# Optimization experiments

Measured on AMD Instinct MI355X. Metric: run time of the kernel, lower is better.

The kernel has to match this reference:

```python
import jax, jax.numpy as jnp
import numpy as np

EPS = 1e-5

def _layernorm(x, g, b):
    m = jnp.mean(x, axis=-1, keepdims=True)
    v = jnp.mean(jnp.square(x - m), axis=-1, keepdims=True)
    return (x - m) * jax.lax.rsqrt(v + EPS) * g + b

def setup_inputs() -> dict:
    key = jax.random.key(0)
    ks = jax.random.split(key, 4)
    B, N, D = 8, 256, 128
    h = jax.random.normal(ks[0], (B, N, D), dtype=jnp.float32)
    adj_J = jax.random.normal(ks[1], (B, N, N), dtype=jnp.float32)
    W_msg = jax.random.normal(ks[2], (D, 2 * D + 1), dtype=jnp.float32) * 0.05
    W_upd = jax.random.normal(ks[3], (D, 2 * D), dtype=jnp.float32) * 0.05
    return {
        "h": h, "adj_J": adj_J,
        "W_msg": W_msg, "b_msg": jnp.zeros((D,), jnp.float32),
        "g_msg": jnp.ones((D,), jnp.float32), "beta_msg": jnp.zeros((D,), jnp.float32),
        "W_upd": W_upd, "b_upd": jnp.zeros((D,), jnp.float32),
        "g_upd": jnp.ones((D,), jnp.float32), "beta_upd": jnp.zeros((D,), jnp.float32),
    }

def reference(h, adj_J, W_msg, b_msg, g_msg, beta_msg, W_upd, b_upd, g_upd, beta_upd):
    B, N, D = h.shape
    # Split msg Linear weight: cat([h_target, h_source, J]) @ W.T is separable.
    Wt = W_msg[:, :D]        # acts on h_target (node i, dim 1)
    Ws = W_msg[:, D:2 * D]   # acts on h_source (node j, dim 2)
    wJ = W_msg[:, 2 * D]     # acts on scalar J
    # pre[b,i,j,e] = h[b,i]@Wt.T + h[b,j]@Ws.T + J[b,i,j]*wJ + b
    pre = (jnp.einsum('bid,ed->bie', h, Wt)[:, :, None, :]
           + jnp.einsum('bjd,ed->bje', h, Ws)[:, None, :, :]
           + adj_J[..., None] * wJ
           + b_msg)
    messages = jax.nn.silu(_layernorm(pre, g_msg, beta_msg))  # (B,N,N,D)
    # mask out self-messages (j == i) then sum over sources j
    idx = jnp.arange(N)
    agg = jnp.sum(messages, axis=2) - messages[:, idx, idx, :]  # (B,N,D)
    upd_pre = (jnp.einsum('bnd,ed->bne', h, W_upd[:, :D])
               + jnp.einsum('bnd,ed->bne', agg, W_upd[:, D:])
               + b_upd)
    dh = jax.nn.silu(_layernorm(upd_pre, g_upd, beta_upd))
    return h + dh
```

## Files before the change

### kernel.cpp

```cpp
#include <hip/hip_runtime.h>

#define BB 8
#define NN 256
#define DD 128
#define SW 257
#define SU 256
#define EPSV 1e-5f

__device__ __forceinline__ float wave_reduce_add(float v) {
#pragma unroll
  for (int off = 32; off > 0; off >>= 1) v += __shfl_xor(v, off, 64);
  return v;
}

__global__ __launch_bounds__(256) void k_proj(
    const float* __restrict__ h, const float* __restrict__ Wm,
    const float* __restrict__ bmsg, const float* __restrict__ Wu,
    float* __restrict__ u, float* __restrict__ s,
    float* __restrict__ rowA, float* __restrict__ rowB,
    float* __restrict__ rowD2, float* __restrict__ rowE2,
    float* __restrict__ wtilv, float* __restrict__ wut) {
  const int blk = blockIdx.x;
  const int b = blk >> 6;
  const int r0 = (blk & 63) * 4;
  const int tid = threadIdx.x;
  const int half = tid >> 7, e = tid & 127;
  const int wv = tid >> 6, lane = tid & 63;

  __shared__ float hs[4][DD];
  __shared__ float pS[4][4], pw[2], pQ[4][4], pD[4][4];

  const float* hb = h + (size_t)(b * NN + r0) * DD;
  if (tid < DD) {
#pragma unroll
    for (int r = 0; r < 4; ++r) hs[r][e] = hb[r * DD + e];
  }
  if (tid >= DD && tid < DD + 64) {
    const int i = blk * 64 + (tid - DD);
    const int d = i >> 7, e2 = i & 127;
    wut[i] = Wu[(size_t)e2 * SU + d];
  }
  __syncthreads();

  float acc[4];
  const float bm = (half == 0) ? bmsg[e] : 0.f;
#pragma unroll
  for (int r = 0; r < 4; ++r) acc[r] = bm;

  const float* wr = Wm + (size_t)e * SW + half * DD;
#pragma unroll 8
  for (int k = 0; k < DD; k += 4) {
    const float4 w4 = *(const float4*)(wr + k);
#pragma unroll
    for (int r = 0; r < 4; ++r) {
      const float4 hv = *(const float4*)(&hs[r][k]);
      acc[r] = fmaf(hv.x, w4.x, acc[r]);
      acc[r] = fmaf(hv.y, w4.y, acc[r]);
      acc[r] = fmaf(hv.z, w4.z, acc[r]);
      acc[r] = fmaf(hv.w, w4.w, acc[r]);
    }
  }

  const float we = Wm[(size_t)e * SW + 2 * DD];
#pragma unroll
  for (int r = 0; r < 4; ++r) {
    const float sm = wave_reduce_add(acc[r]);
    if (lane == 0) pS[wv][r] = sm;
  }
  {
    const float sw = wave_reduce_add(we);
    if (lane == 0 && wv < 2) pw[wv] = sw;
  }
  __syncthreads();

  const int b2 = half * 2;
  const float muw = (pw[0] + pw[1]) * (1.f / DD);
  const float wtil = we - muw;
  float c[4];
#pragma unroll
  for (int r = 0; r < 4; ++r)
    c[r] = acc[r] - (pS[b2][r] + pS[b2 + 1][r]) * (1.f / DD);

  float* outp = (half == 0 ? u : s) + (size_t)(b * NN + r0) * DD;
#pragma unroll
  for (int r = 0; r < 4; ++r) outp[r * DD + e] = c[r];
  if (blk == 0 && half == 0) wtilv[e] = wtil;

#pragma unroll
  for (int r = 0; r < 4; ++r) {
    const float q = wave_reduce_add(c[r] * c[r]);
    const float dd = wave_reduce_add(c[r] * wtil);
    if (lane == 0) { pQ[wv][r] = q; pD[wv][r] = dd; }
  }
  __syncthreads();
  if (tid < 4) {
    const int row = b * NN + r0 + tid;
    rowA[row]  = pQ[0][tid] + pQ[1][tid];
    rowD2[row] = 2.f * (pD[0][tid] + pD[1][tid]);
    rowB[row]  = pQ[2][tid] + pQ[3][tid];
    rowE2[row] = 2.f * (pD[2][tid] + pD[3][tid]);
  }
}

__global__ __launch_bounds__(256) void k_msgfused(
    const float* __restrict__ h, const float* __restrict__ u,
    const float* __restrict__ s, const float* __restrict__ adj,
    const float* __restrict__ rowA, const float* __restrict__ rowB,
    const float* __restrict__ rowD2, const float* __restrict__ rowE2,
    const float* __restrict__ wtilv, const float* __restrict__ g,
    const float* __restrict__ be, const float* __restrict__ wut,
    const float* __restrict__ bu, const float* __restrict__ gu,
    const float* __restrict__ beu, float* __restrict__ out) {
  const int blk = blockIdx.x;
  const int b = blk >> 7, ip = blk & 127;
  const int i0 = 2 * ip, i1 = i0 + 1;
  const int tid = threadIdx.x, lane = tid & 63, wv = tid >> 6;
  const int bNN = b * NN;

  __shared__ __align__(16) float st_[32 * 132];
  __shared__ __align__(16) float upair_[2 * DD];
  __shared__ __align__(16) float hrow_[2 * DD];
  __shared__ float2 pak0[32], pak1[32];
  __shared__ float pm[2][2], pq[2][2];

  {
    const int ii = tid >> 7, e = tid & 127;
    upair_[ii * DD + e] = u[(size_t)(bNN + i0 + ii) * DD + e];
    hrow_[ii * DD + e]  = h[(size_t)(bNN + i0 + ii) * DD + e];
  }
  const float2 wt2 = *(const float2*)(wtilv + 2 * lane);
  const float2 g2  = *(const float2*)(g + 2 * lane);
  const float2 be2 = *(const float2*)(be + 2 * lane);
  const float C = wave_reduce_add(fmaf(wt2.x, wt2.x, wt2.y * wt2.y));
  const float A0 = rowA[bNN + i0], A1 = rowA[bNN + i1];
  const float D20 = rowD2[bNN + i0], D21 = rowD2[bNN + i1];
  __syncthreads();
  const float2 uu0 = *(const float2*)(&upair_[2 * lane]);
  const float2 uu1 = *(const float2*)(&upair_[DD + 2 * lane]);

  float accA0 = 0.f, accA1 = 0.f, accB0 = 0.f, accB1 = 0.f;
  const float* sb = s + (size_t)bNN * DD;

  for (int tile = 0; tile < 8; ++tile) {
    const int t0 = tile * 32;
    __syncthreads();
    {
      const int r = tid >> 5, c4 = (tid & 31) * 4;
#pragma unroll
      for (int p = 0; p < 4; ++p) {
        const int row = p * 8 + r;
        *(float4*)(&st_[row * 132 + c4]) =
            *(const float4*)(sb + (size_t)(t0 + row) * DD + c4);
      }
    }
    __syncthreads();
    {
      const int j = tid >> 3, seg = tid & 7, k0 = seg * 16;
      float d0 = 0.f, d1 = 0.f;
#pragma unroll
      for (int k = 0; k < 16; k += 4) {
        const float4 sv = *(const float4*)(&st_[j * 132 + k0 + k]);
        const float4 u0v = *(const float4*)(&upair_[k0 + k]);
        const float4 u1v = *(const float4*)(&upair_[DD + k0 + k]);
        d0 = fmaf(sv.x, u0v.x, d0); d0 = fmaf(sv.y, u0v.y, d0);
        d0 = fmaf(sv.z, u0v.z, d0); d0 = fmaf(sv.w, u0v.w, d0);
        d1 = fmaf(sv.x, u1v.x, d1); d1 = fmaf(sv.y, u1v.y, d1);
        d1 = fmaf(sv.z, u1v.z, d1); d1 = fmaf(sv.w, u1v.w, d1);
      }
#pragma unroll
      for (int m = 1; m < 8; m <<= 1) {
        d0 += __shfl_xor(d0, m, 64);
        d1 += __shfl_xor(d1, m, 64);
      }
      if (seg == 0) {
        const int jg = t0 + j;
        const float Bj = rowB[bNN + jg], E2j = rowE2[bNN + jg];
        const float a0 = adj[(size_t)(bNN + i0) * NN + jg];
        const float a1 = adj[(size_t)(bNN + i1) * NN + jg];
        const float q0 = fmaf(a0, fmaf(a0, C, D20 + E2j), A0 + Bj + 2.f * d0);
        const float q1 = fmaf(a1, fmaf(a1, C, D21 + E2j), A1 + Bj + 2.f * d1);
        pak0[j] = make_float2(a0, __builtin_amdgcn_rsqf(fmaf(q0, 1.f / DD, EPSV)));
        pak1[j] = make_float2(a1, __builtin_amdgcn_rsqf(fmaf(q1, 1.f / DD, EPSV)));
      }
    }
    __syncthreads();
    for (int jj = wv; jj < 32; jj += 4) {
      const int jg = t0 + jj;
      const float2 ss = *(const float2*)(&st_[jj * 132 + 2 * lane]);
      const float sx0 = uu0.x + ss.x, sx1 = uu0.y + ss.y;
      const float tx0 = uu1.x + ss.x, tx1 = uu1.y + ss.y;
      if (jg != i0) {
        const float2 p = pak0[jj];
        const float x0 = fmaf(p.x, wt2.x, sx0);
        const float x1 = fmaf(p.x, wt2.y, sx1);
        const float y0 = fmaf(x0 * p.y, g2.x, be2.x);
        const float y1 = fmaf(x1 * p.y, g2.y, be2.y);
        accA0 = fmaf(y0, __builtin_amdgcn_rcpf(1.f + __expf(-y0)), accA0);
        accA1 = fmaf(y1, __builtin_amdgcn_rcpf(1.f + __expf(-y1)), accA1);
      }
      if (jg != i1) {
        const float2 p = pak1[jj];
        const float x0 = fmaf(p.x, wt2.x, tx0);
        const float x1 = fmaf(p.x, wt2.y, tx1);
        const float y0 = fmaf(x0 * p.y, g2.x, be2.x);
        const float y1 = fmaf(x1 * p.y, g2.y, be2.y);
        accB0 = fmaf(y0, __builtin_amdgcn_rcpf(1.f + __expf(-y0)), accB0);
        accB1 = fmaf(y1, __builtin_amdgcn_rcpf(1.f + __expf(-y1)), accB1);
      }
    }
  }

  __syncthreads();
  *(float2*)(&st_[(wv * 2 + 0) * DD + 2 * lane]) = make_float2(accA0, accA1);
  *(float2*)(&st_[(wv * 2 + 1) * DD + 2 * lane]) = make_float2(accB0, accB1);
  __syncthreads();
  {
    const int ii = tid >> 7, e = tid & 127;
    st_[(8 + ii) * DD + e] = st_[(0 * 2 + ii) * DD + e] +
                             st_[(1 * 2 + ii) * DD + e] +
                             st_[(2 * 2 + ii) * DD + e] +
                             st_[(3 * 2 + ii) * DD + e];
  }
  __syncthreads();

  const int half = tid >> 7, e = tid & 127;
  float v0 = (half == 0) ? bu[e] : 0.f;
  float v1 = v0;
  {
    const float* xin = (half == 0) ? hrow_ : &st_[8 * DD];
    const float* wcol = wut + (size_t)half * DD * DD + e;
#pragma unroll 8
    for (int k = 0; k < DD; ++k) {
      const float w = wcol[(size_t)k * DD];
      v0 = fmaf(xin[k], w, v0);
      v1 = fmaf(xin[DD + k], w, v1);
    }
  }
  if (half == 1) { upair_[e] = v0; upair_[DD + e] = v1; }
  __syncthreads();
  if (half == 0) {
    v0 += upair_[e];
    v1 += upair_[DD + e];
    const float sm0 = wave_reduce_add(v0), sq0 = wave_reduce_add(v0 * v0);
    const float sm1 = wave_reduce_add(v1), sq1 = wave_reduce_add(v1 * v1);
    if (lane == 0) {
      pm[wv][0] = sm0; pq[wv][0] = sq0;
      pm[wv][1] = sm1; pq[wv][1] = sq1;
    }
  }
  __syncthreads();
  if (half == 0) {
    const float ge = gu[e], bee = beu[e];
    {
      const float mean = (pm[0][0] + pm[1][0]) * (1.f / DD);
      const float var = (pq[0][0] + pq[1][0]) * (1.f / DD) - mean * mean;
      const float rs = __builtin_amdgcn_rsqf(var + EPSV);
      const float y = fmaf((v0 - mean) * rs, ge, bee);
      const float sg = __builtin_amdgcn_rcpf(1.f + __expf(-y));
      out[(size_t)(bNN + i0) * DD + e] = hrow_[e] + y * sg;
    }
    {
      const float mean = (pm[0][1] + pm[1][1]) * (1.f / DD);
      const float var = (pq[0][1] + pq[1][1]) * (1.f / DD) - mean * mean;
      const float rs = __builtin_amdgcn_rsqf(var + EPSV);
      const float y = fmaf((v1 - mean) * rs, ge, bee);
      const float sg = __builtin_amdgcn_rcpf(1.f + __expf(-y));
      out[(size_t)(bNN + i1) * DD + e] = hrow_[DD + e] + y * sg;
    }
  }
}

extern "C" void kernel_launch(void* const* d_in, const int* in_sizes, int n_in,
                              void* d_out, int out_size, void* d_ws, size_t ws_size,
                              hipStream_t stream) {
  const float* h    = (const float*)d_in[0];
  const float* adj  = (const float*)d_in[1];
  const float* Wm   = (const float*)d_in[2];
  const float* bmsg = (const float*)d_in[3];
  const float* gmsg = (const float*)d_in[4];
  const float* bemsg= (const float*)d_in[5];
  const float* Wu   = (const float*)d_in[6];
  const float* bupd = (const float*)d_in[7];
  const float* gupd = (const float*)d_in[8];
  const float* beupd= (const float*)d_in[9];
  float* out = (float*)d_out;

  float* ws    = (float*)d_ws;
  float* u     = ws;
  float* s     = u + BB * NN * DD;
  float* rowA  = s + BB * NN * DD;
  float* rowB  = rowA + BB * NN;
  float* rowD2 = rowB + BB * NN;
  float* rowE2 = rowD2 + BB * NN;
  float* wtilv = rowE2 + BB * NN;
  float* wut   = wtilv + DD;

  k_proj<<<512, 256, 0, stream>>>(h, Wm, bmsg, Wu, u, s, rowA, rowB, rowD2,
                                  rowE2, wtilv, wut);
  k_msgfused<<<1024, 256, 0, stream>>>(h, u, s, adj, rowA, rowB, rowD2, rowE2,
                                       wtilv, gmsg, bemsg, wut, bupd, gupd,
                                       beupd, out);
}
```

Baseline: 56.30 us.

## Double-buffer source tiles with register prefetch in fused message kernel

```diff
diff --git a/kernel.cpp b/kernel.cpp
--- a/kernel.cpp
+++ b/kernel.cpp
@@ -102,7 +102,7 @@
   }
 }
 
-__global__ __launch_bounds__(256) void k_msgfused(
+__global__ __launch_bounds__(256) void k_msgdb(
     const float* __restrict__ h, const float* __restrict__ u,
     const float* __restrict__ s, const float* __restrict__ adj,
     const float* __restrict__ rowA, const float* __restrict__ rowB,
@@ -117,10 +117,10 @@
   const int tid = threadIdx.x, lane = tid & 63, wv = tid >> 6;
   const int bNN = b * NN;
 
-  __shared__ __align__(16) float st_[32 * 132];
+  __shared__ __align__(16) float st_[2][32 * 132];
   __shared__ __align__(16) float upair_[2 * DD];
   __shared__ __align__(16) float hrow_[2 * DD];
-  __shared__ float2 pak0[32], pak1[32];
+  __shared__ float2 pak0[2][32], pak1[2][32];
   __shared__ float pm[2][2], pq[2][2];
 
   {
@@ -138,88 +138,120 @@
   const float2 uu0 = *(const float2*)(&upair_[2 * lane]);
   const float2 uu1 = *(const float2*)(&upair_[DD + 2 * lane]);
 
+  const int j8 = tid >> 3, seg = tid & 7, k0 = seg * 16;
+  const float* srcbase = s + (size_t)(bNN + j8) * DD + k0;
+  float4 ra, rb, rc, rd;
+
+#define DOTS_WRITE(BUF, T) do {                                               \
+    float d0 = 0.f, d1 = 0.f;                                                 \
+    const float4 ua0 = *(const float4*)(&upair_[k0]);                         \
+    const float4 ua1 = *(const float4*)(&upair_[k0 + 4]);                     \
+    const float4 ua2 = *(const float4*)(&upair_[k0 + 8]);                     \
+    const float4 ua3 = *(const float4*)(&upair_[k0 + 12]);                    \
+    const float4 ub0 = *(const float4*)(&upair_[DD + k0]);                    \
+    const float4 ub1 = *(const float4*)(&upair_[DD + k0 + 4]);                \
+    const float4 ub2 = *(const float4*)(&upair_[DD + k0 + 8]);                \
+    const float4 ub3 = *(const float4*)(&upair_[DD + k0 + 12]);               \
+    d0 = fmaf(ra.x, ua0.x, d0); d0 = fmaf(ra.y, ua0.y, d0);                   \
+    d0 = fmaf(ra.z, ua0.z, d0); d0 = fmaf(ra.w, ua0.w, d0);                   \
+    d0 = fmaf(rb.x, ua1.x, d0); d0 = fmaf(rb.y, ua1.y, d0);                   \
+    d0 = fmaf(rb.z, ua1.z, d0); d0 = fmaf(rb.w, ua1.w, d0);                   \
+    d0 = fmaf(rc.x, ua2.x, d0); d0 = fmaf(rc.y, ua2.y, d0);                   \
+    d0 = fmaf(rc.z, ua2.z, d0); d0 = fmaf(rc.w, ua2.w, d0);                   \
+    d0 = fmaf(rd.x, ua3.x, d0); d0 = fmaf(rd.y, ua3.y, d0);                   \
+    d0 = fmaf(rd.z, ua3.z, d0); d0 = fmaf(rd.w, ua3.w, d0);                   \
+    d1 = fmaf(ra.x, ub0.x, d1); d1 = fmaf(ra.y, ub0.y, d1);                   \
+    d1 = fmaf(ra.z, ub0.z, d1); d1 = fmaf(ra.w, ub0.w, d1);                   \
+    d1 = fmaf(rb.x, ub1.x, d1); d1 = fmaf(rb.y, ub1.y, d1);                   \
+    d1 = fmaf(rb.z, ub1.z, d1); d1 = fmaf(rb.w, ub1.w, d1);                   \
+    d1 = fmaf(rc.x, ub2.x, d1); d1 = fmaf(rc.y, ub2.y, d1);                   \
+    d1 = fmaf(rc.z, ub2.z, d1); d1 = fmaf(rc.w, ub2.w, d1);                   \
+    d1 = fmaf(rd.x, ub3.x, d1); d1 = fmaf(rd.y, ub3.y, d1);                   \
+    d1 = fmaf(rd.z, ub3.z, d1); d1 = fmaf(rd.w, ub3.w, d1);                   \
+    float* dst = &st_[BUF][j8 * 132 + k0];                                    \
+    *(float4*)(dst)      = ra; *(float4*)(dst + 4)  = rb;                     \
+    *(float4*)(dst + 8)  = rc; *(float4*)(dst + 12) = rd;                     \
+    d0 += __shfl_xor(d0, 1, 64); d1 += __shfl_xor(d1, 1, 64);                 \
+    d0 += __shfl_xor(d0, 2, 64); d1 += __shfl_xor(d1, 2, 64);                 \
+    d0 += __shfl_xor(d0, 4, 64); d1 += __shfl_xor(d1, 4, 64);                 \
+    if (seg == 0) {                                                           \
+      const int jg = (T) * 32 + j8;                                           \
+      const float Bj = rowB[bNN + jg], E2j = rowE2[bNN + jg];                 \
+      const float a0 = adj[(size_t)(bNN + i0) * NN + jg];                     \
+      const float a1 = adj[(size_t)(bNN + i1) * NN + jg];                     \
+      const float q0 = fmaf(a0, fmaf(a0, C, D20 + E2j), A0 + Bj + 2.f * d0);  \
+      const float q1 = fmaf(a1, fmaf(a1, C, D21 + E2j), A1 + Bj + 2.f * d1);  \
+      pak0[BUF][j8] = make_float2(a0,                                         \
+          __builtin_amdgcn_rsqf(fmaf(q0, 1.f / DD, EPSV)));                   \
+      pak1[BUF][j8] = make_float2(a1,                                         \
+          __builtin_amdgcn_rsqf(fmaf(q1, 1.f / DD, EPSV)));                   \
+    }                                                                         \
+  } while (0)
+
+  {
+    const float* p = srcbase;
+    ra = *(const float4*)(p);     rb = *(const float4*)(p + 4);
+    rc = *(const float4*)(p + 8); rd = *(const float4*)(p + 12);
+  }
+  DOTS_WRITE(0, 0);
+  __syncthreads();
+
   float accA0 = 0.f, accA1 = 0.f, accB0 = 0.f, accB1 = 0.f;
-  const float* sb = s + (size_t)bNN * DD;
-
-  for (int tile = 0; tile < 8; ++tile) {
-    const int t0 = tile * 32;
-    __syncthreads();
+  int cur = 0;
+
+  for (int t = 0; t < 8; ++t) {
+    if (t < 7) {
+      const float* p = srcbase + (size_t)(t + 1) * 32 * DD;
+      ra = *(const float4*)(p);     rb = *(const float4*)(p + 4);
+      rc = *(const float4*)(p + 8); rd = *(const float4*)(p + 12);
+    }
     {
-      const int r = tid >> 5, c4 = (tid & 31) * 4;
-#pragma unroll
-      for (int p = 0; p < 4; ++p) {
-        const int row = p * 8 + r;
-        *(float4*)(&st_[row * 132 + c4]) =
-            *(const float4*)(sb + (size_t)(t0 + row) * DD + c4);
+      const float* stc = st_[cur];
+      const float2* p0 = pak0[cur];
+      const float2* p1 = pak1[cur];
+      const int t0 = t * 32;
+      for (int jj = wv; jj < 32; jj += 4) {
+        const int jg = t0 + jj;
+        const float2 ss = *(const float2*)(&stc[jj * 132 + 2 * lane]);
+        const float sx0 = uu0.x + ss.x, sx1 = uu0.y + ss.y;
+        const float tx0 = uu1.x + ss.x, tx1 = uu1.y + ss.y;
+        if (jg != i0) {
+          const float2 p = p0[jj];
+          const float x0 = fmaf(p.x, wt2.x, sx0);
+          const float x1 = fmaf(p.x, wt2.y, sx1);
+          const float y0 = fmaf(x0 * p.y, g2.x, be2.x);
+          const float y1 = fmaf(x1 * p.y, g2.y, be2.y);
+          accA0 = fmaf(y0, __builtin_amdgcn_rcpf(1.f + __expf(-y0)), accA0);
+          accA1 = fmaf(y1, __builtin_amdgcn_rcpf(1.f + __expf(-y1)), accA1);
+        }
+        if (jg != i1) {
+          const float2 p = p1[jj];
+          const float x0 = fmaf(p.x, wt2.x, tx0);
+          const float x1 = fmaf(p.x, wt2.y, tx1);
+          const float y0 = fmaf(x0 * p.y, g2.x, be2.x);
+          const float y1 = fmaf(x1 * p.y, g2.y, be2.y);
+          accB0 = fmaf(y0, __builtin_amdgcn_rcpf(1.f + __expf(-y0)), accB0);
+          accB1 = fmaf(y1, __builtin_amdgcn_rcpf(1.f + __expf(-y1)), accB1);
+        }
       }
     }
-    __syncthreads();
-    {
-      const int j = tid >> 3, seg = tid & 7, k0 = seg * 16;
-      float d0 = 0.f, d1 = 0.f;
-#pragma unroll
-      for (int k = 0; k < 16; k += 4) {
-        const float4 sv = *(const float4*)(&st_[j * 132 + k0 + k]);
-        const float4 u0v = *(const float4*)(&upair_[k0 + k]);
-        const float4 u1v = *(const float4*)(&upair_[DD + k0 + k]);
-        d0 = fmaf(sv.x, u0v.x, d0); d0 = fmaf(sv.y, u0v.y, d0);
-        d0 = fmaf(sv.z, u0v.z, d0); d0 = fmaf(sv.w, u0v.w, d0);
-        d1 = fmaf(sv.x, u1v.x, d1); d1 = fmaf(sv.y, u1v.y, d1);
-        d1 = fmaf(sv.z, u1v.z, d1); d1 = fmaf(sv.w, u1v.w, d1);
-      }
-#pragma unroll
-      for (int m = 1; m < 8; m <<= 1) {
-        d0 += __shfl_xor(d0, m, 64);
-        d1 += __shfl_xor(d1, m, 64);
-      }
-      if (seg == 0) {
-        const int jg = t0 + j;
-        const float Bj = rowB[bNN + jg], E2j = rowE2[bNN + jg];
-        const float a0 = adj[(size_t)(bNN + i0) * NN + jg];
-        const float a1 = adj[(size_t)(bNN + i1) * NN + jg];
-        const float q0 = fmaf(a0, fmaf(a0, C, D20 + E2j), A0 + Bj + 2.f * d0);
-        const float q1 = fmaf(a1, fmaf(a1, C, D21 + E2j), A1 + Bj + 2.f * d1);
-        pak0[j] = make_float2(a0, __builtin_amdgcn_rsqf(fmaf(q0, 1.f / DD, EPSV)));
-        pak1[j] = make_float2(a1, __builtin_amdgcn_rsqf(fmaf(q1, 1.f / DD, EPSV)));
-      }
-    }
-    __syncthreads();
-    for (int jj = wv; jj < 32; jj += 4) {
-      const int jg = t0 + jj;
-      const float2 ss = *(const float2*)(&st_[jj * 132 + 2 * lane]);
-      const float sx0 = uu0.x + ss.x, sx1 = uu0.y + ss.y;
-      const float tx0 = uu1.x + ss.x, tx1 = uu1.y + ss.y;
-      if (jg != i0) {
-        const float2 p = pak0[jj];
-        const float x0 = fmaf(p.x, wt2.x, sx0);
-        const float x1 = fmaf(p.x, wt2.y, sx1);
-        const float y0 = fmaf(x0 * p.y, g2.x, be2.x);
-        const float y1 = fmaf(x1 * p.y, g2.y, be2.y);
-        accA0 = fmaf(y0, __builtin_amdgcn_rcpf(1.f + __expf(-y0)), accA0);
-        accA1 = fmaf(y1, __builtin_amdgcn_rcpf(1.f + __expf(-y1)), accA1);
-      }
-      if (jg != i1) {
-        const float2 p = pak1[jj];
-        const float x0 = fmaf(p.x, wt2.x, tx0);
-        const float x1 = fmaf(p.x, wt2.y, tx1);
-        const float y0 = fmaf(x0 * p.y, g2.x, be2.x);
-        const float y1 = fmaf(x1 * p.y, g2.y, be2.y);
-        accB0 = fmaf(y0, __builtin_amdgcn_rcpf(1.f + __expf(-y0)), accB0);
-        accB1 = fmaf(y1, __builtin_amdgcn_rcpf(1.f + __expf(-y1)), accB1);
-      }
-    }
-  }
-
-  __syncthreads();
-  *(float2*)(&st_[(wv * 2 + 0) * DD + 2 * lane]) = make_float2(accA0, accA1);
-  *(float2*)(&st_[(wv * 2 + 1) * DD + 2 * lane]) = make_float2(accB0, accB1);
+    if (t < 7) {
+      DOTS_WRITE(cur ^ 1, t + 1);
+      __syncthreads();
+      cur ^= 1;
+    }
+  }
+
+  __syncthreads();
+  *(float2*)(&st_[0][(wv * 2 + 0) * DD + 2 * lane]) = make_float2(accA0, accA1);
+  *(float2*)(&st_[0][(wv * 2 + 1) * DD + 2 * lane]) = make_float2(accB0, accB1);
   __syncthreads();
   {
     const int ii = tid >> 7, e = tid & 127;
-    st_[(8 + ii) * DD + e] = st_[(0 * 2 + ii) * DD + e] +
-                             st_[(1 * 2 + ii) * DD + e] +
-                             st_[(2 * 2 + ii) * DD + e] +
-                             st_[(3 * 2 + ii) * DD + e];
+    st_[0][(8 + ii) * DD + e] = st_[0][(0 + ii) * DD + e] +
+                                st_[0][(2 + ii) * DD + e] +
+                                st_[0][(4 + ii) * DD + e] +
+                                st_[0][(6 + ii) * DD + e];
   }
   __syncthreads();
 
@@ -227,7 +259,7 @@
   float v0 = (half == 0) ? bu[e] : 0.f;
   float v1 = v0;
   {
-    const float* xin = (half == 0) ? hrow_ : &st_[8 * DD];
+    const float* xin = (half == 0) ? hrow_ : &st_[0][8 * DD];
     const float* wcol = wut + (size_t)half * DD * DD + e;
 #pragma unroll 8
     for (int k = 0; k < DD; ++k) {
@@ -297,7 +329,7 @@
 
   k_proj<<<512, 256, 0, stream>>>(h, Wm, bmsg, Wu, u, s, rowA, rowB, rowD2,
                                   rowE2, wtilv, wut);
-  k_msgfused<<<1024, 256, 0, stream>>>(h, u, s, adj, rowA, rowB, rowD2, rowE2,
-                                       wtilv, gmsg, bemsg, wut, bupd, gupd,
-                                       beupd, out);
+  k_msgdb<<<1024, 256, 0, stream>>>(h, u, s, adj, rowA, rowB, rowD2, rowE2,
+                                    wtilv, gmsg, bemsg, wut, bupd, gupd,
+                                    beupd, out);
 }
```

Result: no change. 56.48 us (+0.3%).

## Replace shared-memory tiling of source rows with register prefetch in message kernel

Applied to the files above, without the earlier changes.

```diff
diff --git a/kernel.cpp b/kernel.cpp
--- a/kernel.cpp
+++ b/kernel.cpp
@@ -6,6 +6,8 @@
 #define SW 257
 #define SU 256
 #define EPSV 1e-5f
+#define LOG2E 1.4426950408889634f
+#define LN2F 0.6931471805599453f
 
 __device__ __forceinline__ float wave_reduce_add(float v) {
 #pragma unroll
@@ -102,7 +104,7 @@
   }
 }
 
-__global__ __launch_bounds__(256) void k_msgfused(
+__global__ __launch_bounds__(256) void k_msgreg(
     const float* __restrict__ h, const float* __restrict__ u,
     const float* __restrict__ s, const float* __restrict__ adj,
     const float* __restrict__ rowA, const float* __restrict__ rowB,
@@ -115,12 +117,14 @@
   const int b = blk >> 7, ip = blk & 127;
   const int i0 = 2 * ip, i1 = i0 + 1;
   const int tid = threadIdx.x, lane = tid & 63, wv = tid >> 6;
+  const int seg = lane & 7, jloc = lane >> 3;
+  const int jrow = wv * 8 + jloc;
   const int bNN = b * NN;
 
-  __shared__ __align__(16) float st_[32 * 132];
   __shared__ __align__(16) float upair_[2 * DD];
   __shared__ __align__(16) float hrow_[2 * DD];
-  __shared__ float2 pak0[32], pak1[32];
+  __shared__ __align__(16) float4 pakr_[NN];
+  __shared__ __align__(16) float sacc_[10 * DD];
   __shared__ float pm[2][2], pq[2][2];
 
   {
@@ -128,98 +132,116 @@
     upair_[ii * DD + e] = u[(size_t)(bNN + i0 + ii) * DD + e];
     hrow_[ii * DD + e]  = h[(size_t)(bNN + i0 + ii) * DD + e];
   }
+  pakr_[tid] = make_float4(adj[(size_t)(bNN + i0) * NN + tid],
+                           adj[(size_t)(bNN + i1) * NN + tid],
+                           rowB[bNN + tid], rowE2[bNN + tid]);
   const float2 wt2 = *(const float2*)(wtilv + 2 * lane);
   const float2 g2  = *(const float2*)(g + 2 * lane);
   const float2 be2 = *(const float2*)(be + 2 * lane);
+  const float2 gl2  = make_float2(g2.x * LOG2E, g2.y * LOG2E);
+  const float2 bel2 = make_float2(be2.x * LOG2E, be2.y * LOG2E);
   const float C = wave_reduce_add(fmaf(wt2.x, wt2.x, wt2.y * wt2.y));
   const float A0 = rowA[bNN + i0], A1 = rowA[bNN + i1];
   const float D20 = rowD2[bNN + i0], D21 = rowD2[bNN + i1];
   __syncthreads();
+
   const float2 uu0 = *(const float2*)(&upair_[2 * lane]);
   const float2 uu1 = *(const float2*)(&upair_[DD + 2 * lane]);
+  float4 ua[4], ub[4];
+#pragma unroll
+  for (int c = 0; c < 4; ++c) {
+    ua[c] = *(const float4*)(&upair_[seg * 16 + c * 4]);
+    ub[c] = *(const float4*)(&upair_[DD + seg * 16 + c * 4]);
+  }
+
+  const float* cA_ptr = s + (size_t)(bNN + wv * 8) * DD + 2 * lane;
+  const float* sB_ptr = s + (size_t)(bNN + jrow) * DD + seg * 16;
+
+  float2 colreg[2][8];
+  float4 sreg[4];
+#pragma unroll
+  for (int k = 0; k < 8; ++k)
+    colreg[0][k] = *(const float2*)(cA_ptr + (size_t)k * DD);
+#pragma unroll
+  for (int c = 0; c < 4; ++c)
+    sreg[c] = *(const float4*)(sB_ptr + c * 4);
 
   float accA0 = 0.f, accA1 = 0.f, accB0 = 0.f, accB1 = 0.f;
-  const float* sb = s + (size_t)bNN * DD;
-
-  for (int tile = 0; tile < 8; ++tile) {
-    const int t0 = tile * 32;
-    __syncthreads();
-    {
-      const int r = tid >> 5, c4 = (tid & 31) * 4;
-#pragma unroll
-      for (int p = 0; p < 4; ++p) {
-        const int row = p * 8 + r;
-        *(float4*)(&st_[row * 132 + c4]) =
-            *(const float4*)(sb + (size_t)(t0 + row) * DD + c4);
+
+#pragma unroll
+  for (int t = 0; t < 8; ++t) {
+    float d0 = 0.f, d1 = 0.f;
+#pragma unroll
+    for (int c = 0; c < 4; ++c) {
+      d0 = fmaf(sreg[c].x, ua[c].x, d0); d0 = fmaf(sreg[c].y, ua[c].y, d0);
+      d0 = fmaf(sreg[c].z, ua[c].z, d0); d0 = fmaf(sreg[c].w, ua[c].w, d0);
+      d1 = fmaf(sreg[c].x, ub[c].x, d1); d1 = fmaf(sreg[c].y, ub[c].y, d1);
+      d1 = fmaf(sreg[c].z, ub[c].z, d1); d1 = fmaf(sreg[c].w, ub[c].w, d1);
+    }
+    d0 += __shfl_xor(d0, 1, 64); d1 += __shfl_xor(d1, 1, 64);
+    d0 += __shfl_xor(d0, 2, 64); d1 += __shfl_xor(d1, 2, 64);
+    d0 += __shfl_xor(d0, 4, 64); d1 += __shfl_xor(d1, 4, 64);
+
+    const int jgq = t * 32 + jrow;
+    const float4 pk = pakr_[jgq];
+    const float q0 = fmaf(pk.x, fmaf(pk.x, C, D20 + pk.w), A0 + pk.z + 2.f * d0);
+    const float q1 = fmaf(pk.y, fmaf(pk.y, C, D21 + pk.w), A1 + pk.z + 2.f * d1);
+    const float rs0v = __builtin_amdgcn_rsqf(fmaf(q0, 1.f / DD, EPSV));
+    const float rs1v = __builtin_amdgcn_rsqf(fmaf(q1, 1.f / DD, EPSV));
+    const float a0v = pk.x, a1v = pk.y;
+
+    if (t < 7) {
+#pragma unroll
+      for (int c = 0; c < 4; ++c)
+        sreg[c] = *(const float4*)(sB_ptr + (size_t)(t + 1) * 32 * DD + c * 4);
+#pragma unroll
+      for (int k = 0; k < 8; ++k)
+        colreg[(t + 1) & 1][k] =
+            *(const float2*)(cA_ptr + (size_t)((t + 1) * 32 + k) * DD);
+    }
+
+#pragma unroll
+    for (int k = 0; k < 8; ++k) {
+      const float rs0k = __shfl(rs0v, k * 8, 64);
+      const float rs1k = __shfl(rs1v, k * 8, 64);
+      const float a0k = __shfl(a0v, k * 8, 64);
+      const float a1k = __shfl(a1v, k * 8, 64);
+      const int jgk = t * 32 + wv * 8 + k;
+      const float2 ss = colreg[t & 1][k];
+      const float s0x = uu0.x + ss.x, s0y = uu0.y + ss.y;
+      const float s1x = uu1.x + ss.x, s1y = uu1.y + ss.y;
+      if (jgk != i0) {
+        const float x0 = fmaf(a0k, wt2.x, s0x);
+        const float x1 = fmaf(a0k, wt2.y, s0y);
+        const float z0 = fmaf(x0 * rs0k, gl2.x, bel2.x);
+        const float z1 = fmaf(x1 * rs0k, gl2.y, bel2.y);
+        const float e0 = exp2f(-z0), e1 = exp2f(-z1);
+        accA0 = fmaf(z0, __builtin_amdgcn_rcpf(1.f + e0), accA0);
+        accA1 = fmaf(z1, __builtin_amdgcn_rcpf(1.f + e1), accA1);
       }
-    }
-    __syncthreads();
-    {
-      const int j = tid >> 3, seg = tid & 7, k0 = seg * 16;
-      float d0 = 0.f, d1 = 0.f;
-#pragma unroll
-      for (int k = 0; k < 16; k += 4) {
-        const float4 sv = *(const float4*)(&st_[j * 132 + k0 + k]);
-        const float4 u0v = *(const float4*)(&upair_[k0 + k]);
-        const float4 u1v = *(const float4*)(&upair_[DD + k0 + k]);
-        d0 = fmaf(sv.x, u0v.x, d0); d0 = fmaf(sv.y, u0v.y, d0);
-        d0 = fmaf(sv.z, u0v.z, d0); d0 = fmaf(sv.w, u0v.w, d0);
-        d1 = fmaf(sv.x, u1v.x, d1); d1 = fmaf(sv.y, u1v.y, d1);
-        d1 = fmaf(sv.z, u1v.z, d1); d1 = fmaf(sv.w, u1v.w, d1);
+      if (jgk != i1) {
+        const float x0 = fmaf(a1k, wt2.x, s1x);
+        const float x1 = fmaf(a1k, wt2.y, s1y);
+        const float z0 = fmaf(x0 * rs1k, gl2.x, bel2.x);
+        const float z1 = fmaf(x1 * rs1k, gl2.y, bel2.y);
+        const float e0 = exp2f(-z0), e1 = exp2f(-z1);
+        accB0 = fmaf(z0, __builtin_amdgcn_rcpf(1.f + e0), accB0);
+        accB1 = fmaf(z1, __builtin_amdgcn_rcpf(1.f + e1), accB1);
       }
-#pragma unroll
-      for (int m = 1; m < 8; m <<= 1) {
-        d0 += __shfl_xor(d0, m, 64);
-        d1 += __shfl_xor(d1, m, 64);
-      }
-      if (seg == 0) {
-        const int jg = t0 + j;
-        const float Bj = rowB[bNN + jg], E2j = rowE2[bNN + jg];
-        const float a0 = adj[(size_t)(bNN + i0) * NN + jg];
-        const float a1 = adj[(size_t)(bNN + i1) * NN + jg];
-        const float q0 = fmaf(a0, fmaf(a0, C, D20 + E2j), A0 + Bj + 2.f * d0);
-        const float q1 = fmaf(a1, fmaf(a1, C, D21 + E2j), A1 + Bj + 2.f * d1);
-        pak0[j] = make_float2(a0, __builtin_amdgcn_rsqf(fmaf(q0, 1.f / DD, EPSV)));
-        pak1[j] = make_float2(a1, __builtin_amdgcn_rsqf(fmaf(q1, 1.f / DD, EPSV)));
-      }
-    }
-    __syncthreads();
-    for (int jj = wv; jj < 32; jj += 4) {
-      const int jg = t0 + jj;
-      const float2 ss = *(const float2*)(&st_[jj * 132 + 2 * lane]);
-      const float sx0 = uu0.x + ss.x, sx1 = uu0.y + ss.y;
-      const float tx0 = uu1.x + ss.x, tx1 = uu1.y + ss.y;
-      if (jg != i0) {
-        const float2 p = pak0[jj];
-        const float x0 = fmaf(p.x, wt2.x, sx0);
-        const float x1 = fmaf(p.x, wt2.y, sx1);
-        const float y0 = fmaf(x0 * p.y, g2.x, be2.x);
-        const float y1 = fmaf(x1 * p.y, g2.y, be2.y);
-        accA0 = fmaf(y0, __builtin_amdgcn_rcpf(1.f + __expf(-y0)), accA0);
-        accA1 = fmaf(y1, __builtin_amdgcn_rcpf(1.f + __expf(-y1)), accA1);
-      }
-      if (jg != i1) {
-        const float2 p = pak1[jj];
-        const float x0 = fmaf(p.x, wt2.x, tx0);
-        const float x1 = fmaf(p.x, wt2.y, tx1);
-        const float y0 = fmaf(x0 * p.y, g2.x, be2.x);
-        const float y1 = fmaf(x1 * p.y, g2.y, be2.y);
-        accB0 = fmaf(y0, __builtin_amdgcn_rcpf(1.f + __expf(-y0)), accB0);
-        accB1 = fmaf(y1, __builtin_amdgcn_rcpf(1.f + __expf(-y1)), accB1);
-      }
-    }
-  }
-
-  __syncthreads();
-  *(float2*)(&st_[(wv * 2 + 0) * DD + 2 * lane]) = make_float2(accA0, accA1);
-  *(float2*)(&st_[(wv * 2 + 1) * DD + 2 * lane]) = make_float2(accB0, accB1);
+    }
+  }
+
+  *(float2*)(&sacc_[(wv * 2 + 0) * DD + 2 * lane]) =
+      make_float2(accA0 * LN2F, accA1 * LN2F);
+  *(float2*)(&sacc_[(wv * 2 + 1) * DD + 2 * lane]) =
+      make_float2(accB0 * LN2F, accB1 * LN2F);
   __syncthreads();
   {
     const int ii = tid >> 7, e = tid & 127;
-    st_[(8 + ii) * DD + e] = st_[(0 * 2 + ii) * DD + e] +
-                             st_[(1 * 2 + ii) * DD + e] +
-                             st_[(2 * 2 + ii) * DD + e] +
-                             st_[(3 * 2 + ii) * DD + e];
+    sacc_[(8 + ii) * DD + e] = sacc_[(0 + ii) * DD + e] +
+                               sacc_[(2 + ii) * DD + e] +
+                               sacc_[(4 + ii) * DD + e] +
+                               sacc_[(6 + ii) * DD + e];
   }
   __syncthreads();
 
@@ -227,7 +249,7 @@
   float v0 = (half == 0) ? bu[e] : 0.f;
   float v1 = v0;
   {
-    const float* xin = (half == 0) ? hrow_ : &st_[8 * DD];
+    const float* xin = (half == 0) ? hrow_ : &sacc_[8 * DD];
     const float* wcol = wut + (size_t)half * DD * DD + e;
 #pragma unroll 8
     for (int k = 0; k < DD; ++k) {
@@ -297,7 +319,7 @@
 
   k_proj<<<512, 256, 0, stream>>>(h, Wm, bmsg, Wu, u, s, rowA, rowB, rowD2,
                                   rowE2, wtilv, wut);
-  k_msgfused<<<1024, 256, 0, stream>>>(h, u, s, adj, rowA, rowB, rowD2, rowE2,
-                                       wtilv, gmsg, bemsg, wut, bupd, gupd,
-                                       beupd, out);
+  k_msgreg<<<1024, 256, 0, stream>>>(h, u, s, adj, rowA, rowB, rowD2, rowE2,
+                                     wtilv, gmsg, bemsg, wut, bupd, gupd,
+                                     beupd, out);
 }
```

Measured after the change: 56.71 us. Within noise of the previous version (+0.7%).
